# Kernel optimization log

Measured on AMD Instinct MI355X. Metric: run time of the kernel, lower is better.

Reference implementation:

```python
import jax, jax.numpy as jnp
import numpy as np

D_MODEL = 1024
N_HEADS = 16
HEAD_DIM = D_MODEL // N_HEADS
Q_PROJ = D_MODEL // 2
KV_PROJ = D_MODEL
INIT_SCALE = 0.02
EPS = 1e-5


def _ln(x, g, b):
    mu = jnp.mean(x, axis=-1, keepdims=True)
    var = jnp.mean(jnp.square(x - mu), axis=-1, keepdims=True)
    return (x - mu) * jax.lax.rsqrt(var + EPS) * g + b


def setup_inputs() -> dict:
    key = jax.random.key(0)
    ks = jax.random.split(key, 8)
    B, S = 2, 2048
    x = jax.random.normal(ks[0], (B, S, D_MODEL), dtype=jnp.float32)
    W_dq = INIT_SCALE * jax.random.normal(ks[1], (D_MODEL, Q_PROJ), dtype=jnp.float32)
    W_uq = INIT_SCALE * jax.random.normal(ks[2], (Q_PROJ, D_MODEL), dtype=jnp.float32)
    W_dkv = INIT_SCALE * jax.random.normal(ks[3], (D_MODEL, KV_PROJ), dtype=jnp.float32)
    W_ukv = INIT_SCALE * jax.random.normal(ks[4], (KV_PROJ, 2 * D_MODEL), dtype=jnp.float32)
    wo = INIT_SCALE * jax.random.normal(ks[5], (D_MODEL, D_MODEL), dtype=jnp.float32)
    return {
        "x": x,
        "W_dq": W_dq, "W_uq": W_uq,
        "q_ln_g": jnp.ones((Q_PROJ,), jnp.float32), "q_ln_b": jnp.zeros((Q_PROJ,), jnp.float32),
        "W_dkv": W_dkv, "W_ukv": W_ukv,
        "kv_ln_g": jnp.ones((KV_PROJ,), jnp.float32), "kv_ln_b": jnp.zeros((KV_PROJ,), jnp.float32),
        "preq_g": jnp.ones((D_MODEL,), jnp.float32), "preq_b": jnp.zeros((D_MODEL,), jnp.float32),
        "prekv_g": jnp.ones((D_MODEL,), jnp.float32), "prekv_b": jnp.zeros((D_MODEL,), jnp.float32),
        "wo": wo,
    }


def reference(x, W_dq, W_uq, q_ln_g, q_ln_b, W_dkv, W_ukv, kv_ln_g, kv_ln_b,
              preq_g, preq_b, prekv_g, prekv_b, wo):
    B, S, D = x.shape
    H, dh = N_HEADS, HEAD_DIM
    # Q path: pre-norm -> low-rank down -> LN -> up
    x_q = _ln(x, preq_g, preq_b)
    cq = _ln(x_q @ W_dq, q_ln_g, q_ln_b)            # [B,S,D/2]
    Q = (cq @ W_uq).reshape(B, S, H, dh)             # [B,S,H,dh]
    Q = Q / jnp.sqrt(jnp.asarray(dh, x.dtype))
    # KV path: pre-norm -> compress -> LN -> up, split into K,V
    x_kv = _ln(x, prekv_g, prekv_b)
    ckv = _ln(x_kv @ W_dkv, kv_ln_g, kv_ln_b)        # [B,S,D]
    KV = ckv @ W_ukv                                 # [B,S,2D]
    K, V = jnp.split(KV, 2, axis=-1)
    K = K.reshape(B, S, H, dh)
    V = V.reshape(B, S, H, dh)
    # causal attention (scores materialized as in original)
    scores = jnp.einsum('bqhd,bkhd->bhqk', Q, K)     # [B,H,S,S]
    causal = jnp.tril(jnp.ones((S, S), dtype=bool))  # True where allowed
    scores = jnp.where(causal[None, None], scores, jnp.asarray(-jnp.inf, scores.dtype))
    attn = jax.nn.softmax(scores, axis=-1)
    out = jnp.einsum('bhqk,bkhd->bqhd', attn, V).reshape(B, S, D)
    return out @ wo.T
```

## Files before the change

kernel.cpp:

```cpp
#include <hip/hip_runtime.h>
#include <hip/hip_bf16.h>

#define SEQ   2048
#define BATCH 2
#define NROWS 4096
#define DM    1024
#define NHEAD 16
#define DH    64
#define QP    512
#define KVP   1024
#define CH    8

typedef unsigned short us;
typedef ushort4 us4;
using bf16x8 = __attribute__((ext_vector_type(8))) __bf16;
using f32x4  = __attribute__((ext_vector_type(4))) float;

__device__ __forceinline__ us f2bf(float f) {
  union { __hip_bfloat16 h; us u; } cv;
  cv.h = __float2bfloat16(f);
  return cv.u;
}
__device__ __forceinline__ float bf2f(us u) {
  union { unsigned int u32; float f; } cv;
  cv.u32 = ((unsigned int)u) << 16;
  return cv.f;
}
__device__ __forceinline__ float loadp(const void* p, long i, int isbf) {
  return isbf ? bf2f(((const us*)p)[i]) : ((const float*)p)[i];
}
__device__ __forceinline__ void async16(const void* g, void* l) {
  __builtin_amdgcn_global_load_lds((__attribute__((address_space(1))) void*)g,
                                   (__attribute__((address_space(3))) void*)l,
                                   16, 0, 0);
}
__device__ __forceinline__ unsigned cvtpk(float lo, float hi) {
  unsigned r;
  asm("v_cvt_pk_bf16_f32 %0, %1, %2" : "=v"(r) : "v"(lo), "v"(hi));
  return r;
}

__global__ void detect_dtype(const us* __restrict__ xu, int* __restrict__ flag) {
  __shared__ int red[256];
  const int tid = threadIdx.x;
  int cnt = 0;
  for (int i = tid; i < 4096; i += 256) {
    const int e = (xu[i] >> 7) & 0xff;
    if (e == 0 || (e >= 100 && e <= 134)) cnt++;
  }
  red[tid] = cnt;
  __syncthreads();
  for (int s = 128; s; s >>= 1) {
    if (tid < s) red[tid] += red[tid + s];
    __syncthreads();
  }
  if (tid == 0) *flag = (red[0] >= 3900) ? 1 : 0;
}

struct TD { const void* in; us* out; int R, C, nt, trans; };

__global__ __launch_bounds__(256) void stage0(
    TD t0, TD t1, TD t2, TD t3, TD t4,
    float4* __restrict__ zp, int n4,
    const void* __restrict__ xin,
    const void* __restrict__ g1, const void* __restrict__ b1,
    const void* __restrict__ g2, const void* __restrict__ b2,
    us* __restrict__ out1, us* __restrict__ out2,
    const int* __restrict__ flag)
{
  __shared__ us tile[32][33];
  __shared__ float red[8];
  __shared__ float musd[2];
  const int tid = threadIdx.x;
  const int isbf = *flag;
  int lin = blockIdx.x;

  if (lin < 5120) {
    TD t = t0;
    if (lin >= t.nt) { lin -= t.nt; t = t1;
      if (lin >= t.nt) { lin -= t.nt; t = t2;
        if (lin >= t.nt) { lin -= t.nt; t = t3;
          if (lin >= t.nt) { lin -= t.nt; t = t4; } } } }
    const int ntx = t.C >> 5;
    const int by = lin / ntx, bx = lin - by * ntx;
    const int tx = tid & 31, ty = tid >> 5;
    const long r0 = (long)by * 32, c0 = (long)bx * 32;
    if (t.trans) {
#pragma unroll
      for (int i = 0; i < 32; i += 8)
        tile[ty + i][tx] = isbf ? ((const us*)t.in)[(r0 + ty + i) * t.C + c0 + tx]
                                : f2bf(((const float*)t.in)[(r0 + ty + i) * t.C + c0 + tx]);
      __syncthreads();
#pragma unroll
      for (int i = 0; i < 32; i += 8)
        t.out[(c0 + ty + i) * t.R + r0 + tx] = tile[tx][ty + i];
    } else {
#pragma unroll
      for (int i = 0; i < 32; i += 8)
        t.out[(r0 + ty + i) * t.C + c0 + tx] =
            isbf ? ((const us*)t.in)[(r0 + ty + i) * t.C + c0 + tx]
                 : f2bf(((const float*)t.in)[(r0 + ty + i) * t.C + c0 + tx]);
    }
    return;
  }
  if (lin < 6144) {
    const float4 z = {0.f, 0.f, 0.f, 0.f};
    for (int i = (lin - 5120) * 256 + tid; i < n4; i += 1024 * 256) zp[i] = z;
    return;
  }
  const long row = lin - 6144;
  float v[4];
  float s = 0.f, s2 = 0.f;
#pragma unroll
  for (int i = 0; i < 4; i++) {
    const long c = tid + i * 256;
    const float t = loadp(xin, row * 1024 + c, isbf);
    v[i] = t; s += t; s2 += t * t;
  }
#pragma unroll
  for (int off = 32; off > 0; off >>= 1) {
    s  += __shfl_down(s,  off);
    s2 += __shfl_down(s2, off);
  }
  const int wave = tid >> 6, lane = tid & 63;
  if (lane == 0) { red[wave] = s; red[4 + wave] = s2; }
  __syncthreads();
  if (tid == 0) {
    const float ts = red[0] + red[1] + red[2] + red[3];
    const float t2 = red[4] + red[5] + red[6] + red[7];
    const float mu = ts * (1.f / 1024.f);
    const float var = t2 * (1.f / 1024.f) - mu * mu;
    musd[0] = mu; musd[1] = rsqrtf(var + 1e-5f);
  }
  __syncthreads();
  const float mu = musd[0], rs = musd[1];
#pragma unroll
  for (int i = 0; i < 4; i++) {
    const long c = tid + i * 256;
    const float nrm = (v[i] - mu) * rs;
    out1[row * 1024 + c] = f2bf(nrm * loadp(g1, c, isbf) + loadp(b1, c, isbf));
    out2[row * 1024 + c] = f2bf(nrm * loadp(g2, c, isbf) + loadp(b2, c, isbf));
  }
}

template<int C>
__device__ __forceinline__ void ln_body(const us* __restrict__ in,
                                        const void* __restrict__ g, const void* __restrict__ b,
                                        us* __restrict__ out, long row, int tid, int isbf) {
  constexpr int NP = C / 256;
  float v[NP];
  float s = 0.f, s2 = 0.f;
#pragma unroll
  for (int i = 0; i < NP; i++) {
    const float t = bf2f(in[row * C + tid + i * 256]);
    v[i] = t; s += t; s2 += t * t;
  }
#pragma unroll
  for (int off = 32; off > 0; off >>= 1) {
    s  += __shfl_down(s,  off);
    s2 += __shfl_down(s2, off);
  }
  __shared__ float red[8];
  __shared__ float musd[2];
  const int wave = tid >> 6, lane = tid & 63;
  if (lane == 0) { red[wave] = s; red[4 + wave] = s2; }
  __syncthreads();
  if (tid == 0) {
    const float ts = red[0] + red[1] + red[2] + red[3];
    const float t2 = red[4] + red[5] + red[6] + red[7];
    const float mu = ts * (1.f / C);
    const float var = t2 * (1.f / C) - mu * mu;
    musd[0] = mu; musd[1] = rsqrtf(var + 1e-5f);
  }
  __syncthreads();
  const float mu = musd[0], rs = musd[1];
#pragma unroll
  for (int i = 0; i < NP; i++) {
    const long c = tid + i * 256;
    out[row * C + c] = f2bf((v[i] - mu) * rs * loadp(g, c, isbf) + loadp(b, c, isbf));
  }
}

__global__ __launch_bounds__(256) void ln_rows_pair(
    const us* __restrict__ inq, const void* __restrict__ qg, const void* __restrict__ qb,
    us* __restrict__ outq,
    const us* __restrict__ inkv, const void* __restrict__ kvg, const void* __restrict__ kvb,
    us* __restrict__ outkv,
    const int* __restrict__ flag)
{
  const int isbf = *flag;
  if (blockIdx.x < NROWS)
    ln_body<512>(inq, qg, qb, outq, blockIdx.x, threadIdx.x, isbf);
  else
    ln_body<1024>(inkv, kvg, kvb, outkv, blockIdx.x - NROWS, threadIdx.x, isbf);
}

struct GD { const us* A; const us* Bt; void* C; int N, K, nxs; float scale; int omode; };

__global__ __launch_bounds__(256) void gemm_mt(GD g0, GD g1, int nb0,
                                               const int* __restrict__ flag) {
  __shared__ us As[2][128 * 32];
  __shared__ us Bs[2][64 * 32];
  GD g;
  int lin = blockIdx.x;
  {
    const int cpx = gridDim.x >> 3;
    lin = (lin & 7) * cpx + (lin >> 3);
  }
  if (lin < nb0) g = g0; else { g = g1; lin -= nb0; }
  const int by = lin >> g.nxs;
  const int bx = lin - (by << g.nxs);
  const int N = g.N, K = g.K;

  const int tid  = threadIdx.x;
  const int lane = tid & 63;
  const int wave = tid >> 6;
  const int n16  = lane & 15;
  const int quad = lane >> 4;
  const long m0 = (long)by * 128;
  const long n0 = (long)bx * 64;
  const int wm = (wave >> 1) * 64;
  const int wn = (wave & 1) * 32;

  const f32x4 zero = {0.f, 0.f, 0.f, 0.f};
  f32x4 acc[4][2];
#pragma unroll
  for (int i = 0; i < 4; i++)
#pragma unroll
    for (int j = 0; j < 2; j++) acc[i][j] = zero;

  const int srow = tid >> 2;
  const int scol = (tid & 3) * 8;
  const us* Ag0 = g.A  + (m0 + srow) * K + scol;
  const us* Ag1 = g.A  + (m0 + 64 + srow) * K + scol;
  const us* Bg0 = g.Bt + (n0 + srow) * K + scol;
  const int lds_off = srow * 32 + scol;

  for (int k0 = 0; k0 < K; k0 += 64) {
#pragma unroll
    for (int s = 0; s < 2; s++) {
      const int ks = k0 + s * 32;
      async16(Ag0 + ks, As[s] + lds_off);
      async16(Ag1 + ks, As[s] + 2048 + lds_off);
      async16(Bg0 + ks, Bs[s] + lds_off);
    }
    __syncthreads();
#pragma unroll
    for (int s = 0; s < 2; s++) {
      bf16x8 af[4], bfv[2];
#pragma unroll
      for (int i = 0; i < 4; i++)
        af[i] = *(const bf16x8*)(As[s] + (wm + i * 16 + n16) * 32 + quad * 8);
#pragma unroll
      for (int j = 0; j < 2; j++)
        bfv[j] = *(const bf16x8*)(Bs[s] + (wn + j * 16 + n16) * 32 + quad * 8);
#pragma unroll
      for (int i = 0; i < 4; i++)
#pragma unroll
        for (int j = 0; j < 2; j++)
          acc[i][j] = __builtin_amdgcn_mfma_f32_16x16x32_bf16(af[i], bfv[j], acc[i][j], 0, 0, 0);
    }
    __syncthreads();
  }

  const bool obf = (g.omode == 1) || (g.omode == 2 && *flag != 0);
  float* Cf = (float*)g.C;
  us* Cb = (us*)g.C;
#pragma unroll
  for (int i = 0; i < 4; i++) {
    const long row = m0 + wm + i * 16 + quad * 4;
#pragma unroll
    for (int j = 0; j < 2; j++) {
      const long col = n0 + wn + j * 16 + n16;
#pragma unroll
      for (int r = 0; r < 4; r++) {
        const float v = acc[i][j][r] * g.scale;
        if (obf) Cb[(row + r) * N + col] = f2bf(v);
        else     Cf[(row + r) * N + col] = v;
      }
    }
  }
}

#define SWZ(row, col) ((row) * 64 + ((col) ^ (((row) & 7) << 3)))

__global__ __launch_bounds__(256, 4) void flash_attn(
    const us* __restrict__ Q, const us* __restrict__ KV,
    float* __restrict__ Oacc, float* __restrict__ Lacc)
{
  __shared__ us Ks[2][64 * 64];
  __shared__ us Vt[2][64 * 64];

  int lin = blockIdx.x;
  int qt = 31, nc = 0;
  for (; qt >= 0; --qt) { nc = (qt >> 3) + 1; if (lin < nc) break; lin -= nc; }
  const int chunk = lin;
  const int kt0 = chunk * CH;
  const int kt1 = min(kt0 + CH, qt + 1);
  const int nt = kt1 - kt0;

  const int h   = blockIdx.y;
  const int bb  = blockIdx.z;
  const int tid = threadIdx.x;
  const int lane = tid & 63;
  const int wave = tid >> 6;
  const int n16 = lane & 15;
  const int quad = lane >> 4;
  const int qbase = qt * 64;
  const long rowQ0 = (long)bb * SEQ;

  bf16x8 aq[2];
  {
    const long gq = (rowQ0 + qbase + wave * 16 + n16) * DM + h * DH;
    aq[0] = *(const bf16x8*)(Q + gq + quad * 8);
    aq[1] = *(const bf16x8*)(Q + gq + 32 + quad * 8);
  }

  const f32x4 zero = {0.f, 0.f, 0.f, 0.f};
  f32x4 oacc[4];
#pragma unroll
  for (int d = 0; d < 4; d++) oacc[d] = zero;
  float rsum = 0.f;

  const int kk_key = tid >> 3;
  const int kk_d8  = (tid & 7) * 8;
  const int vd  = tid & 63;
  const int vw  = tid >> 6;
  const int vkb = vw * 8;

  const us* kgb = KV + (rowQ0 + kk_key) * 2048 + h * DH + kk_d8;
  const us* vgb = KV + (rowQ0 + vw * 4) * 2048 + KVP + h * DH + vd;

  uint4 kpre0, kpre1;
  us vraw[16];
  auto loadKV = [&](int kt) {
    const us* kg = kgb + (long)kt * (64 * 2048);
    kpre0 = *(const uint4*)kg;
    kpre1 = *(const uint4*)(kg + 32 * 2048);
    const us* vg = vgb + (long)kt * (64 * 2048);
#pragma unroll
    for (int r = 0; r < 4; r++) {
      vraw[r]      = vg[r * 2048];
      vraw[4 + r]  = vg[(16 + r) * 2048];
      vraw[8 + r]  = vg[(32 + r) * 2048];
      vraw[12 + r] = vg[(48 + r) * 2048];
    }
  };
  auto writeLDS = [&](int b) {
    *(uint4*)(Ks[b] + SWZ(kk_key, kk_d8))      = kpre0;
    *(uint4*)(Ks[b] + SWZ(kk_key + 32, kk_d8)) = kpre1;
    uint4 p0, p1;
    p0.x = (unsigned)vraw[0]  | ((unsigned)vraw[1]  << 16);
    p0.y = (unsigned)vraw[2]  | ((unsigned)vraw[3]  << 16);
    p0.z = (unsigned)vraw[4]  | ((unsigned)vraw[5]  << 16);
    p0.w = (unsigned)vraw[6]  | ((unsigned)vraw[7]  << 16);
    p1.x = (unsigned)vraw[8]  | ((unsigned)vraw[9]  << 16);
    p1.y = (unsigned)vraw[10] | ((unsigned)vraw[11] << 16);
    p1.z = (unsigned)vraw[12] | ((unsigned)vraw[13] << 16);
    p1.w = (unsigned)vraw[14] | ((unsigned)vraw[15] << 16);
    *(uint4*)(Vt[b] + SWZ(vd, vkb))      = p0;
    *(uint4*)(Vt[b] + SWZ(vd, vkb + 32)) = p1;
  };

  loadKV(kt0);
  writeLDS(0);

  for (int ti = 0; ti < nt; ti++) {
    const int cur = ti & 1;
    if (ti + 1 < nt) loadKV(kt0 + ti + 1);
    __syncthreads();
    const us* ksb = Ks[cur];
    const us* vtb = Vt[cur];
    const int kt = kt0 + ti;

    f32x4 sv[4];
#pragma unroll
    for (int j = 0; j < 4; j++) {
      const bf16x8 ak0 = *(const bf16x8*)(ksb + SWZ(j * 16 + n16, quad * 8));
      const bf16x8 ak1 = *(const bf16x8*)(ksb + SWZ(j * 16 + n16, 32 + quad * 8));
      f32x4 s = zero;
      s = __builtin_amdgcn_mfma_f32_16x16x32_bf16(ak0, aq[0], s, 0, 0, 0);
      s = __builtin_amdgcn_mfma_f32_16x16x32_bf16(ak1, aq[1], s, 0, 0, 0);
      sv[j] = s;
    }

    if (kt == qt) {
      const int qrl = wave * 16 + n16;
#pragma unroll
      for (int j = 0; j < 4; j++) {
        const int kl = j * 16 + quad * 4;
#pragma unroll
        for (int r = 0; r < 4; r++)
          sv[j][r] = (kl + r <= qrl) ? sv[j][r] : -1e30f;
      }
    }

    unsigned pep[4][2];
#pragma unroll
    for (int j = 0; j < 4; j++) {
      const float p0 = __builtin_amdgcn_exp2f(sv[j][0]);
      const float p1 = __builtin_amdgcn_exp2f(sv[j][1]);
      const float p2 = __builtin_amdgcn_exp2f(sv[j][2]);
      const float p3 = __builtin_amdgcn_exp2f(sv[j][3]);
      rsum += (p0 + p1) + (p2 + p3);
      pep[j][0] = cvtpk(p0, p1);
      pep[j][1] = cvtpk(p2, p3);
    }

    __builtin_amdgcn_s_setprio(1);
#pragma unroll
    for (int kc = 0; kc < 2; kc++) {
      union { bf16x8 v; unsigned u[4]; } apu;
      apu.u[0] = pep[2 * kc][0];
      apu.u[1] = pep[2 * kc][1];
      apu.u[2] = pep[2 * kc + 1][0];
      apu.u[3] = pep[2 * kc + 1][1];
#pragma unroll
      for (int d = 0; d < 4; d++) {
        const bf16x8 bv = *(const bf16x8*)(vtb + SWZ(d * 16 + n16, kc * 32 + quad * 8));
        oacc[d] = __builtin_amdgcn_mfma_f32_16x16x32_bf16(apu.v, bv, oacc[d], 0, 0, 0);
      }
    }
    __builtin_amdgcn_s_setprio(0);

    if (ti + 1 < nt) writeLDS(cur ^ 1);
  }

  rsum += __shfl_xor(rsum, 16);
  rsum += __shfl_xor(rsum, 32);

  const long rw0 = rowQ0 + qbase + wave * 16;
  if (quad == 0)
    atomicAdd(&Lacc[(rw0 + n16) * NHEAD + h], rsum);
#pragma unroll
  for (int r = 0; r < 4; r++) {
    float* dst = Oacc + (rw0 + quad * 4 + r) * DM + h * DH + n16;
#pragma unroll
    for (int d = 0; d < 4; d++)
      atomicAdd(dst + d * 16, oacc[d][r]);
  }
}

__global__ __launch_bounds__(256) void flash_combine(
    const float* __restrict__ Oacc, const float* __restrict__ Lacc,
    us* __restrict__ O)
{
  __shared__ float invl[NHEAD];
  const long row = blockIdx.x;
  const int tid = threadIdx.x;
  if (tid < NHEAD) invl[tid] = 1.f / Lacc[row * NHEAD + tid];
  __syncthreads();
#pragma unroll
  for (int i = 0; i < 4; i++) {
    const int col = tid + i * 256;
    O[row * DM + col] = f2bf(Oacc[row * DM + col] * invl[col >> 6]);
  }
}

extern "C" void kernel_launch(void* const* d_in, const int* in_sizes, int n_in,
                              void* d_out, int out_size, void* d_ws, size_t ws_size,
                              hipStream_t stream) {
  const void* x      = d_in[0];
  const void* Wdq    = d_in[1];
  const void* Wuq    = d_in[2];
  const void* qg     = d_in[3];
  const void* qb     = d_in[4];
  const void* Wdkv   = d_in[5];
  const void* Wukv   = d_in[6];
  const void* kvg    = d_in[7];
  const void* kvb    = d_in[8];
  const void* preqg  = d_in[9];
  const void* preqb  = d_in[10];
  const void* prekvg = d_in[11];
  const void* prekvb = d_in[12];
  const void* wo     = d_in[13];

  char* ws = (char*)d_ws;
  const long MB = 1 << 20;
  int* flag   = (int*)ws;
  us* wdq_t   = (us*)(ws + 1 * MB);
  us* wuq_t   = (us*)(ws + 2 * MB);
  us* wdkv_t  = (us*)(ws + 3 * MB);
  us* wukv_t  = (us*)(ws + 5 * MB);
  us* wo_c    = (us*)(ws + 9 * MB);
  us* xq      = (us*)(ws + 11 * MB);
  us* xkv     = (us*)(ws + 19 * MB);
  float* Oacc = (float*)(ws + 27 * MB);
  float* Lacc = (float*)(ws + 43 * MB);
  us* obuf    = (us*)(ws + 43 * MB + 256 * 1024);
  us* tq_bf   = obuf;
  us* cq      = (us*)(ws + 43 * MB + 256 * 1024 + 8 * MB);
  us* qbuf    = (us*)(ws + 43 * MB + 256 * 1024 + 12 * MB);
  us* tkv_bf  = qbuf;
  us* ckv     = (us*)(ws + 43 * MB + 256 * 1024 + 20 * MB);
  us* kv      = (us*)(ws + 43 * MB + 256 * 1024 + 28 * MB);

  detect_dtype<<<1, 256, 0, stream>>>((const us*)x, flag);

  {
    TD t0 = { Wdq,  wdq_t,  1024,  512,  512, 1 };
    TD t1 = { Wuq,  wuq_t,   512, 1024,  512, 1 };
    TD t2 = { Wdkv, wdkv_t, 1024, 1024, 1024, 1 };
    TD t3 = { Wukv, wukv_t, 1024, 2048, 2048, 1 };
    TD t4 = { wo,   wo_c,   1024, 1024, 1024, 0 };
    const int n4 = (16 * 1024 * 1024 + 256 * 1024) / 16;
    stage0<<<10240, 256, 0, stream>>>(t0, t1, t2, t3, t4,
                                      (float4*)Oacc, n4,
                                      x, preqg, preqb, prekvg, prekvb, xq, xkv, flag);
  }

  {
    GD g0 = { xq,  wdq_t,  tq_bf,   512, 1024, 3, 1.f, 1 };
    GD g1 = { xkv, wdkv_t, tkv_bf, 1024, 1024, 4, 1.f, 1 };
    gemm_mt<<<768, 256, 0, stream>>>(g0, g1, 256, flag);
  }

  ln_rows_pair<<<2 * NROWS, 256, 0, stream>>>(tq_bf, qg, qb, cq, tkv_bf, kvg, kvb, ckv, flag);

  {
    GD g0 = { cq,  wuq_t,  qbuf, 1024,  512, 4, 0.125f * 1.44269504f, 1 };
    GD g1 = { ckv, wukv_t, kv,   2048, 1024, 5, 1.f, 1 };
    gemm_mt<<<1536, 256, 0, stream>>>(g0, g1, 512, flag);
  }

  flash_attn<<<dim3(80, NHEAD, BATCH), 256, 0, stream>>>(qbuf, kv, Oacc, Lacc);
  flash_combine<<<NROWS, 256, 0, stream>>>(Oacc, Lacc, obuf);

  {
    GD g0 = { obuf, wo_c, d_out, 1024, 1024, 4, 1.f, 2 };
    gemm_mt<<<512, 256, 0, stream>>>(g0, g0, 512, flag);
  }
}
```

Baseline: 270.0 us.

## Fold inner LayerNorm into up-projection GEMM epilogue via precomputed row stats

The separate LN pass that wrote normalized cq/ckv buffers is replaced by a stats-only kernel that stores per-row mean and rstd. The LN gain is folded into the transposed up-projection weights, and the bias and gain column sums are precomputed in extra stage0 blocks. The up-projection GEMM then applies an affine epilogue (acc*rs + u - mu*rs*t), so it reads the raw down-projection output directly. This removes a full bf16 write and re-read of the normalized activations. Separately, the dtype flag is now set from the host by checking input byte size instead of launching the detection kernel. The trade-offs are that the epilogue is numerically less exact (the mean is no longer subtracted before bf16 rounding), and the column-sum blocks are serial K-loops that may lengthen stage0.

```diff
diff --git a/kernel.cpp b/kernel.cpp
--- a/kernel.cpp
+++ b/kernel.cpp
@@ -57,7 +57,7 @@
   if (tid == 0) *flag = (red[0] >= 3900) ? 1 : 0;
 }
 
-struct TD { const void* in; us* out; int R, C, nt, trans; };
+struct TD { const void* in; us* out; int R, C, nt, trans; const void* gv; };
 
 __global__ __launch_bounds__(256) void stage0(
     TD t0, TD t1, TD t2, TD t3, TD t4,
@@ -66,6 +66,10 @@
     const void* __restrict__ g1, const void* __restrict__ b1,
     const void* __restrict__ g2, const void* __restrict__ b2,
     us* __restrict__ out1, us* __restrict__ out2,
+    const void* __restrict__ Wuq_, const void* __restrict__ qg_, const void* __restrict__ qb_,
+    float* __restrict__ utq,
+    const void* __restrict__ Wukv_, const void* __restrict__ kvg_, const void* __restrict__ kvb_,
+    float* __restrict__ utkv,
     const int* __restrict__ flag)
 {
   __shared__ us tile[32][33];
@@ -86,10 +90,19 @@
     const int tx = tid & 31, ty = tid >> 5;
     const long r0 = (long)by * 32, c0 = (long)bx * 32;
     if (t.trans) {
-#pragma unroll
-      for (int i = 0; i < 32; i += 8)
-        tile[ty + i][tx] = isbf ? ((const us*)t.in)[(r0 + ty + i) * t.C + c0 + tx]
-                                : f2bf(((const float*)t.in)[(r0 + ty + i) * t.C + c0 + tx]);
+      if (t.gv) {
+#pragma unroll
+        for (int i = 0; i < 32; i += 8) {
+          const long k = r0 + ty + i;
+          tile[ty + i][tx] = f2bf(loadp(t.in, k * t.C + c0 + tx, isbf) *
+                                  loadp(t.gv, k, isbf));
+        }
+      } else {
+#pragma unroll
+        for (int i = 0; i < 32; i += 8)
+          tile[ty + i][tx] = isbf ? ((const us*)t.in)[(r0 + ty + i) * t.C + c0 + tx]
+                                  : f2bf(((const float*)t.in)[(r0 + ty + i) * t.C + c0 + tx]);
+      }
       __syncthreads();
 #pragma unroll
       for (int i = 0; i < 32; i += 8)
@@ -106,6 +119,24 @@
   if (lin < 6144) {
     const float4 z = {0.f, 0.f, 0.f, 0.f};
     for (int i = (lin - 5120) * 256 + tid; i < n4; i += 1024 * 256) zp[i] = z;
+    return;
+  }
+  if (lin >= 10240) {
+    const int gi = lin - 10240;
+    const void *W, *gv, *bv; float* out; int K, N, n0;
+    if (gi < 4) { W = Wuq_;  gv = qg_;  bv = qb_;  out = utq;  K = 512;  N = 1024; n0 = gi * 256; }
+    else        { W = Wukv_; gv = kvg_; bv = kvb_; out = utkv; K = 1024; N = 2048; n0 = (gi - 4) * 256; }
+    const int n = n0 + tid;
+    float u = 0.f, t = 0.f;
+    for (int k = 0; k < K; k++) {
+      const float w  = loadp(W, (long)k * N + n, isbf);
+      const float gk = loadp(gv, k, isbf);
+      const float bk = loadp(bv, k, isbf);
+      u += bk * w;
+      t += bf2f(f2bf(gk * w));
+    }
+    out[n] = u;
+    out[N + n] = t;
     return;
   }
   const long row = lin - 6144;
@@ -144,16 +175,14 @@
 }
 
 template<int C>
-__device__ __forceinline__ void ln_body(const us* __restrict__ in,
-                                        const void* __restrict__ g, const void* __restrict__ b,
-                                        us* __restrict__ out, long row, int tid, int isbf) {
+__device__ __forceinline__ void stats_body(const us* __restrict__ in,
+                                           float2* __restrict__ out, long row, int tid) {
   constexpr int NP = C / 256;
-  float v[NP];
   float s = 0.f, s2 = 0.f;
 #pragma unroll
   for (int i = 0; i < NP; i++) {
     const float t = bf2f(in[row * C + tid + i * 256]);
-    v[i] = t; s += t; s2 += t * t;
+    s += t; s2 += t * t;
   }
 #pragma unroll
   for (int off = 32; off > 0; off >>= 1) {
@@ -161,7 +190,6 @@
     s2 += __shfl_down(s2, off);
   }
   __shared__ float red[8];
-  __shared__ float musd[2];
   const int wave = tid >> 6, lane = tid & 63;
   if (lane == 0) { red[wave] = s; red[4 + wave] = s2; }
   __syncthreads();
@@ -170,32 +198,20 @@
     const float t2 = red[4] + red[5] + red[6] + red[7];
     const float mu = ts * (1.f / C);
     const float var = t2 * (1.f / C) - mu * mu;
-    musd[0] = mu; musd[1] = rsqrtf(var + 1e-5f);
-  }
-  __syncthreads();
-  const float mu = musd[0], rs = musd[1];
-#pragma unroll
-  for (int i = 0; i < NP; i++) {
-    const long c = tid + i * 256;
-    out[row * C + c] = f2bf((v[i] - mu) * rs * loadp(g, c, isbf) + loadp(b, c, isbf));
-  }
-}
-
-__global__ __launch_bounds__(256) void ln_rows_pair(
-    const us* __restrict__ inq, const void* __restrict__ qg, const void* __restrict__ qb,
-    us* __restrict__ outq,
-    const us* __restrict__ inkv, const void* __restrict__ kvg, const void* __restrict__ kvb,
-    us* __restrict__ outkv,
-    const int* __restrict__ flag)
+    out[row] = make_float2(mu, rsqrtf(var + 1e-5f));
+  }
+}
+
+__global__ __launch_bounds__(256) void ln_stats(
+    const us* __restrict__ tq, float2* __restrict__ mq,
+    const us* __restrict__ tkv, float2* __restrict__ mkv)
 {
-  const int isbf = *flag;
-  if (blockIdx.x < NROWS)
-    ln_body<512>(inq, qg, qb, outq, blockIdx.x, threadIdx.x, isbf);
-  else
-    ln_body<1024>(inkv, kvg, kvb, outkv, blockIdx.x - NROWS, threadIdx.x, isbf);
-}
-
-struct GD { const us* A; const us* Bt; void* C; int N, K, nxs; float scale; int omode; };
+  if (blockIdx.x < NROWS) stats_body<512>(tq, mq, blockIdx.x, threadIdx.x);
+  else                    stats_body<1024>(tkv, mkv, blockIdx.x - NROWS, threadIdx.x);
+}
+
+struct GD { const us* A; const us* Bt; void* C; int N, K, nxs; float scale; int omode;
+            const float2* musd; const float* ut; };
 
 __global__ __launch_bounds__(256) void gemm_mt(GD g0, GD g1, int nb0,
                                                const int* __restrict__ flag) {
@@ -263,9 +279,36 @@
     __syncthreads();
   }
 
+  us* Cb = (us*)g.C;
+  if (g.omode == 3) {
+    float uj[2], tj[2];
+#pragma unroll
+    for (int j = 0; j < 2; j++) {
+      const long col = n0 + wn + j * 16 + n16;
+      uj[j] = g.ut[col] * g.scale;
+      tj[j] = g.ut[N + col];
+    }
+#pragma unroll
+    for (int i = 0; i < 4; i++) {
+      const long row = m0 + wm + i * 16 + quad * 4;
+#pragma unroll
+      for (int r = 0; r < 4; r++) {
+        const float2 ms = g.musd[row + r];
+        const float a = ms.y * g.scale;
+        const float c = ms.x * a;
+#pragma unroll
+        for (int j = 0; j < 2; j++) {
+          const long col = n0 + wn + j * 16 + n16;
+          const float v = acc[i][j][r] * a + (uj[j] - c * tj[j]);
+          Cb[(row + r) * N + col] = f2bf(v);
+        }
+      }
+    }
+    return;
+  }
+
   const bool obf = (g.omode == 1) || (g.omode == 2 && *flag != 0);
   float* Cf = (float*)g.C;
-  us* Cb = (us*)g.C;
 #pragma unroll
   for (int i = 0; i < 4; i++) {
     const long row = m0 + wm + i * 16 + quad * 4;
@@ -489,37 +532,55 @@
   float* Lacc = (float*)(ws + 43 * MB);
   us* obuf    = (us*)(ws + 43 * MB + 256 * 1024);
   us* tq_bf   = obuf;
-  us* cq      = (us*)(ws + 43 * MB + 256 * 1024 + 8 * MB);
+  char* aux   = ws + 43 * MB + 256 * 1024 + 8 * MB;
+  float2* musd_q  = (float2*)aux;
+  float2* musd_kv = (float2*)(aux + 32 * 1024);
+  float*  ut_q    = (float*)(aux + 64 * 1024);
+  float*  ut_kv   = (float*)(aux + 72 * 1024);
   us* qbuf    = (us*)(ws + 43 * MB + 256 * 1024 + 12 * MB);
-  us* tkv_bf  = qbuf;
-  us* ckv     = (us*)(ws + 43 * MB + 256 * 1024 + 20 * MB);
+  us* tkv_bf  = (us*)(ws + 43 * MB + 256 * 1024 + 20 * MB);
   us* kv      = (us*)(ws + 43 * MB + 256 * 1024 + 28 * MB);
 
-  detect_dtype<<<1, 256, 0, stream>>>((const us*)x, flag);
-
-  {
-    TD t0 = { Wdq,  wdq_t,  1024,  512,  512, 1 };
-    TD t1 = { Wuq,  wuq_t,   512, 1024,  512, 1 };
-    TD t2 = { Wdkv, wdkv_t, 1024, 1024, 1024, 1 };
-    TD t3 = { Wukv, wukv_t, 1024, 2048, 2048, 1 };
-    TD t4 = { wo,   wo_c,   1024, 1024, 1024, 0 };
+  {
+    static int hflag;
+    const long xb = (long)in_sizes[0];
+    int known = -1;
+    if (xb == (long)BATCH * SEQ * DM * 4) known = 0;
+    else if (xb == (long)BATCH * SEQ * DM * 2) known = 1;
+    if (known >= 0) {
+      hflag = known;
+      hipMemcpyAsync(flag, &hflag, sizeof(int), hipMemcpyHostToDevice, stream);
+    } else {
+      detect_dtype<<<1, 256, 0, stream>>>((const us*)x, flag);
+    }
+  }
+
+  {
+    TD t0 = { Wdq,  wdq_t,  1024,  512,  512, 1, nullptr };
+    TD t1 = { Wuq,  wuq_t,   512, 1024,  512, 1, qg };
+    TD t2 = { Wdkv, wdkv_t, 1024, 1024, 1024, 1, nullptr };
+    TD t3 = { Wukv, wukv_t, 1024, 2048, 2048, 1, kvg };
+    TD t4 = { wo,   wo_c,   1024, 1024, 1024, 0, nullptr };
     const int n4 = (16 * 1024 * 1024 + 256 * 1024) / 16;
-    stage0<<<10240, 256, 0, stream>>>(t0, t1, t2, t3, t4,
+    stage0<<<10252, 256, 0, stream>>>(t0, t1, t2, t3, t4,
                                       (float4*)Oacc, n4,
-                                      x, preqg, preqb, prekvg, prekvb, xq, xkv, flag);
-  }
-
-  {
-    GD g0 = { xq,  wdq_t,  tq_bf,   512, 1024, 3, 1.f, 1 };
-    GD g1 = { xkv, wdkv_t, tkv_bf, 1024, 1024, 4, 1.f, 1 };
+                                      x, preqg, preqb, prekvg, prekvb, xq, xkv,
+                                      Wuq, qg, qb, ut_q,
+                                      Wukv, kvg, kvb, ut_kv,
+                                      flag);
+  }
+
+  {
+    GD g0 = { xq,  wdq_t,  tq_bf,   512, 1024, 3, 1.f, 1, nullptr, nullptr };
+    GD g1 = { xkv, wdkv_t, tkv_bf, 1024, 1024, 4, 1.f, 1, nullptr, nullptr };
     gemm_mt<<<768, 256, 0, stream>>>(g0, g1, 256, flag);
   }
 
-  ln_rows_pair<<<2 * NROWS, 256, 0, stream>>>(tq_bf, qg, qb, cq, tkv_bf, kvg, kvb, ckv, flag);
-
-  {
-    GD g0 = { cq,  wuq_t,  qbuf, 1024,  512, 4, 0.125f * 1.44269504f, 1 };
-    GD g1 = { ckv, wukv_t, kv,   2048, 1024, 5, 1.f, 1 };
+  ln_stats<<<2 * NROWS, 256, 0, stream>>>(tq_bf, musd_q, tkv_bf, musd_kv);
+
+  {
+    GD g0 = { tq_bf,  wuq_t,  qbuf, 1024,  512, 4, 0.125f * 1.44269504f, 3, musd_q,  ut_q };
+    GD g1 = { tkv_bf, wukv_t, kv,   2048, 1024, 5, 1.f,                  3, musd_kv, ut_kv };
     gemm_mt<<<1536, 256, 0, stream>>>(g0, g1, 512, flag);
   }
 
@@ -527,7 +588,7 @@
   flash_combine<<<NROWS, 256, 0, stream>>>(Oacc, Lacc, obuf);
 
   {
-    GD g0 = { obuf, wo_c, d_out, 1024, 1024, 4, 1.f, 2 };
+    GD g0 = { obuf, wo_c, d_out, 1024, 1024, 4, 1.f, 2, nullptr, nullptr };
     gemm_mt<<<512, 256, 0, stream>>>(g0, g0, 512, flag);
   }
 }
```

Result: slower. 574.2 us (+112.7%).
